# Performance work log

Measured on AMD Instinct MI355X. Metric: run time of the kernel, lower is better.

## Reference

```python
import jax, jax.numpy as jnp
import numpy as np

BN_EPS = 1e-5


def _gru(x, Wih, Whh, bih, bhh):
    # x: [B,S,D]; Wih: [3H,D]; Whh: [3H,H]; PyTorch gate order (r, z, n)
    B, S, D = x.shape
    H = Whh.shape[1]
    xg = jnp.einsum('bsd,gd->bsg', x, Wih) + bih  # [B,S,3H] precomputed input gates

    def step(h, xg_t):
        hg = h @ Whh.T + bhh
        xr, xz, xn = jnp.split(xg_t, 3, axis=-1)
        hr, hz, hn = jnp.split(hg, 3, axis=-1)
        r = jax.nn.sigmoid(xr + hr)
        z = jax.nn.sigmoid(xz + hz)
        n = jnp.tanh(xn + r * hn)
        h_new = (1.0 - z) * n + z * h
        return h_new, h_new

    h0 = jnp.zeros((B, H), x.dtype)
    _, hs = jax.lax.scan(step, h0, jnp.swapaxes(xg, 0, 1))  # [S,B,H]
    return jnp.swapaxes(hs, 0, 1)


def _lstm(x, Wih, Whh, bih, bhh):
    # x: [B,S,D]; PyTorch gate order (i, f, g, o)
    B, S, D = x.shape
    H = Whh.shape[1]
    xg = jnp.einsum('bsd,gd->bsg', x, Wih) + bih  # [B,S,4H]

    def step(carry, xg_t):
        h, c = carry
        g = xg_t + h @ Whh.T + bhh
        i, f, gg, o = jnp.split(g, 4, axis=-1)
        i = jax.nn.sigmoid(i)
        f = jax.nn.sigmoid(f)
        gg = jnp.tanh(gg)
        o = jax.nn.sigmoid(o)
        c_new = f * c + i * gg
        h_new = o * jnp.tanh(c_new)
        return (h_new, c_new), h_new

    h0 = jnp.zeros((B, H), x.dtype)
    c0 = jnp.zeros((B, H), x.dtype)
    _, hs = jax.lax.scan(step, (h0, c0), jnp.swapaxes(xg, 0, 1))
    return jnp.swapaxes(hs, 0, 1)


def setup_inputs() -> dict:
    key = jax.random.key(0)
    B, S, D, H = 64, 512, 40, 512
    ks = jax.random.split(key, 16)
    s_in = 1.0 / np.sqrt(H)

    def u(k, shape):
        return jax.random.uniform(k, shape, jnp.float32, -s_in, s_in)

    inp = {
        'x': jax.random.normal(ks[0], (B, S, D), jnp.float32),
        # rec1: GRU
        'gru_Wih': u(ks[1], (3 * H, D)),
        'gru_Whh': u(ks[2], (3 * H, H)),
        'gru_bih': u(ks[3], (3 * H,)),
        'gru_bhh': u(ks[4], (3 * H,)),
        # rec2: LSTM over [x, ssr] -> input D+1
        'lstm_Wih': u(ks[5], (4 * H, D + 1)),
        'lstm_Whh': u(ks[6], (4 * H, H)),
        'lstm_bih': u(ks[7], (4 * H,)),
        'lstm_bhh': u(ks[8], (4 * H,)),
        # fc1/fc2/fc3: hidden -> 1
        'fc1_w': u(ks[9], (1, H)), 'fc1_b': u(ks[10], (1,)),
        'fc2_w': u(ks[11], (1, H)), 'fc2_b': u(ks[12], (1,)),
        'fc3_w': u(ks[13], (1, H)), 'fc3_b': u(ks[14], (1,)),
        # BatchNorm1d affine params
        'bn_gamma': jnp.ones((H,), jnp.float32),
        'bn_beta': jnp.zeros((H,), jnp.float32),
    }
    return inp


def reference(x, gru_Wih, gru_Whh, gru_bih, gru_bhh,
              lstm_Wih, lstm_Whh, lstm_bih, lstm_bhh,
              fc1_w, fc1_b, fc2_w, fc2_b, fc3_w, fc3_b,
              bn_gamma, bn_beta):
    B, S, D = x.shape
    o1 = _gru(x, gru_Wih, gru_Whh, gru_bih, gru_bhh)  # [B,S,H]
    # BatchNorm1d (training mode): per-channel stats over (batch, time)
    mean = jnp.mean(o1, axis=(0, 1))
    var = jnp.mean((o1 - mean) ** 2, axis=(0, 1))
    o1 = (o1 - mean) * jax.lax.rsqrt(var + BN_EPS) * bn_gamma + bn_beta
    # gated scalar channel (dropout p=0 is identity)
    sr = jax.nn.relu(o1 @ fc1_w.T + fc1_b)            # [B,S,1]
    w = jnp.abs(jax.nn.sigmoid(o1 @ fc2_w.T + fc2_b))  # [B,S,1]
    ssr = sr * (w + 1.0)                              # [B,S,1]
    x2 = jnp.concatenate([x, ssr], axis=2)            # [B,S,D+1]
    o2 = _lstm(x2, lstm_Wih, lstm_Whh, lstm_bih, lstm_bhh)
    out = jax.nn.relu(o2 @ fc3_w.T + fc3_b)           # [B,S,1]
    return out, ssr
```

## Files before the change

### kernel.cpp

```cpp
#include <hip/hip_runtime.h>
#include <stdint.h>

#define MB 16
#define GW 16
#define NU 32
#define HD 512
#define SEQ 512
#define DX 40

using short8 = __attribute__((ext_vector_type(8))) short;
using f32x4  = __attribute__((ext_vector_type(4))) float;
typedef unsigned long long ull;

__device__ __forceinline__ unsigned short f2bf(float f) {
  uint32_t u = __builtin_bit_cast(uint32_t, f);
  u += 0x7fffu + ((u >> 16) & 1u);
  return (unsigned short)(u >> 16);
}
__device__ __forceinline__ float sigm(float x) { return 1.0f / (1.0f + __expf(-x)); }


__global__ __launch_bounds__(512, 2) void gru_kernel(
    const float* __restrict__ x, const float* __restrict__ Wih,
    const float* __restrict__ Whh, const float* __restrict__ bih,
    const float* __restrict__ bhh, unsigned* __restrict__ flags,
    unsigned short* __restrict__ hbuf, float* __restrict__ o1,
    float* __restrict__ stats)
{
  const int wg = blockIdx.x & (GW - 1);
  const int g  = blockIdx.x >> 4;
  const int tid = threadIdx.x;
  const int wave = tid >> 6;
  const int lane = tid & 63;
  const int u0 = wg * NU;
  const int bg = g * MB;

  __shared__ __attribute__((aligned(16))) unsigned short h_s[MB][520];
  __shared__ __attribute__((aligned(16))) unsigned short x_s[MB][72];
  __shared__ float gate_s[3][MB][NU];
  __shared__ float xn_s[MB][NU];

  for (int i = tid; i < MB * 32; i += 512) x_s[i >> 5][40 + (i & 31)] = 0;

  short8 bfrag[18];
  const int myGate = wave >> 1;
  const int ut = wave & 1;
  const int kq = (lane >> 4) * 8;
  if (wave < 6) {
    const int row = myGate * HD + u0 + ut * 16 + (lane & 15);
    for (int kt = 0; kt < 16; ++kt) {
      const float* p = Whh + (size_t)row * HD + kt * 32 + kq;
      short8 f;
#pragma unroll
      for (int j = 0; j < 8; ++j) f[j] = (short)f2bf(p[j]);
      bfrag[kt] = f;
    }
    for (int kt = 16; kt < 18; ++kt) {
      short8 f;
#pragma unroll
      for (int j = 0; j < 8; ++j) {
        int c = kt * 32 + kq + j - HD;
        float v = (myGate < 2 && c < DX) ? Wih[(size_t)row * DX + c] : 0.0f;
        f[j] = (short)f2bf(v);
      }
      bfrag[kt] = f;
    }
  } else {
    const int row = 2 * HD + u0 + (wave - 6) * 16 + (lane & 15);
    for (int kt = 0; kt < 2; ++kt) {
      short8 f;
#pragma unroll
      for (int j = 0; j < 8; ++j) {
        int c = kt * 32 + kq + j;
        f[j] = (short)((c < DX) ? f2bf(Wih[(size_t)row * DX + c]) : 0);
      }
      bfrag[kt] = f;
    }
  }

  const int sb = tid >> 5;
  const int su = tid & 31;
  const int cb = tid & 31;
  float hprev = 0.0f, ssum = 0.0f, ssq = 0.0f;
  const float b_r  = bih[u0 + su] + bhh[u0 + su];
  const float b_z  = bih[HD + u0 + su] + bhh[HD + u0 + su];
  const float b_in = bih[2 * HD + u0 + su];
  const float b_hn = bhh[2 * HD + u0 + su];

  unsigned* gflags = flags + g * 128 * 16;
  unsigned* myflag = gflags + (wg * 8 + wave) * 16;
  unsigned* pollflag = gflags + (((cb >> 1) * 8) + (sb >> 1)) * 16;

  for (int t = 0; t < SEQ; ++t) {
    const ull* hin64 = (const ull*)(hbuf + ((size_t)g * 2 + (t & 1)) * MB * HD);
    uint32_t* hout32 =
        (uint32_t*)(hbuf + ((size_t)g * 2 + ((t + 1) & 1)) * MB * HD);

    const float* xr = x + ((size_t)(bg + sb) * SEQ + t) * DX;
    float xv0 = xr[su];
    float xv1 = (su < 8) ? xr[32 + su] : 0.0f;

    {
      int spin = 0;
      while (__hip_atomic_load(pollflag, __ATOMIC_RELAXED,
                               __HIP_MEMORY_SCOPE_AGENT) < (unsigned)t)
        if (++spin > 2) __builtin_amdgcn_s_sleep(1);
      ull w0 = __hip_atomic_load(hin64 + sb * 128 + cb * 4 + 0, __ATOMIC_RELAXED,
                                 __HIP_MEMORY_SCOPE_AGENT);
      ull w1 = __hip_atomic_load(hin64 + sb * 128 + cb * 4 + 1, __ATOMIC_RELAXED,
                                 __HIP_MEMORY_SCOPE_AGENT);
      ull w2 = __hip_atomic_load(hin64 + sb * 128 + cb * 4 + 2, __ATOMIC_RELAXED,
                                 __HIP_MEMORY_SCOPE_AGENT);
      ull w3 = __hip_atomic_load(hin64 + sb * 128 + cb * 4 + 3, __ATOMIC_RELAXED,
                                 __HIP_MEMORY_SCOPE_AGENT);
      *(ull*)(&h_s[sb][cb * 16 + 0])  = w0;
      *(ull*)(&h_s[sb][cb * 16 + 4])  = w1;
      *(ull*)(&h_s[sb][cb * 16 + 8])  = w2;
      *(ull*)(&h_s[sb][cb * 16 + 12]) = w3;
    }
    x_s[sb][su] = f2bf(xv0);
    if (su < 8) x_s[sb][32 + su] = f2bf(xv1);
    __syncthreads();

    if (wave < 6) {
      const int m = lane & 15;
      f32x4 acc = {0.f, 0.f, 0.f, 0.f};
#pragma unroll
      for (int kt = 0; kt < 16; ++kt) {
        short8 av = *(const short8*)(&h_s[m][kt * 32 + kq]);
        acc = __builtin_amdgcn_mfma_f32_16x16x32_bf16(av, bfrag[kt], acc, 0, 0, 0);
      }
      short8 ax0 = *(const short8*)(&x_s[m][kq]);
      short8 ax1 = *(const short8*)(&x_s[m][32 + kq]);
      acc = __builtin_amdgcn_mfma_f32_16x16x32_bf16(ax0, bfrag[16], acc, 0, 0, 0);
      acc = __builtin_amdgcn_mfma_f32_16x16x32_bf16(ax1, bfrag[17], acc, 0, 0, 0);
#pragma unroll
      for (int r = 0; r < 4; ++r)
        gate_s[myGate][(lane >> 4) * 4 + r][ut * 16 + (lane & 15)] = acc[r];
    } else {
      const int m = lane & 15;
      f32x4 acc = {0.f, 0.f, 0.f, 0.f};
      short8 ax0 = *(const short8*)(&x_s[m][kq]);
      short8 ax1 = *(const short8*)(&x_s[m][32 + kq]);
      acc = __builtin_amdgcn_mfma_f32_16x16x32_bf16(ax0, bfrag[0], acc, 0, 0, 0);
      acc = __builtin_amdgcn_mfma_f32_16x16x32_bf16(ax1, bfrag[1], acc, 0, 0, 0);
#pragma unroll
      for (int r = 0; r < 4; ++r)
        xn_s[(lane >> 4) * 4 + r][(wave - 6) * 16 + (lane & 15)] = acc[r];
    }
    __syncthreads();

    float r_ = sigm(gate_s[0][sb][su] + b_r);
    float z_ = sigm(gate_s[1][sb][su] + b_z);
    float n_ = tanhf(xn_s[sb][su] + b_in + r_ * (gate_s[2][sb][su] + b_hn));
    float h = (1.0f - z_) * n_ + z_ * hprev;
    hprev = h;
    ssum += h; ssq += h * h;
    {
      float hp = __shfl_xor(h, 1);
      if ((tid & 1) == 0) {
        uint32_t packed = (uint32_t)f2bf(h) | ((uint32_t)f2bf(hp) << 16);
        __hip_atomic_store(hout32 + ((sb * HD + u0 + su) >> 1), packed,
                           __ATOMIC_RELAXED, __HIP_MEMORY_SCOPE_AGENT);
      }
      asm volatile("s_waitcnt vmcnt(0)" ::: "memory");
      if (lane == 0)
        __hip_atomic_store(myflag, (unsigned)(t + 1), __ATOMIC_RELAXED,
                           __HIP_MEMORY_SCOPE_AGENT);
    }
    o1[((size_t)(bg + sb) * SEQ + t) * HD + u0 + su] = h;
  }

  atomicAdd(&stats[u0 + su], ssum);
  atomicAdd(&stats[HD + u0 + su], ssq);
}

__global__ __launch_bounds__(512, 2) void lstm_kernel(
    const float* __restrict__ x, const float* __restrict__ Wih,
    const float* __restrict__ Whh, const float* __restrict__ bih,
    const float* __restrict__ bhh, const float* __restrict__ ssr,
    unsigned* __restrict__ flags, unsigned short* __restrict__ hbuf,
    float* __restrict__ o2)
{
  const int wg = blockIdx.x & (GW - 1);
  const int g  = blockIdx.x >> 4;
  const int tid = threadIdx.x;
  const int wave = tid >> 6;
  const int lane = tid & 63;
  const int u0 = wg * NU;
  const int bg = g * MB;

  __shared__ __attribute__((aligned(16))) unsigned short h_s[MB][520];
  __shared__ __attribute__((aligned(16))) unsigned short x_s[MB][72];
  __shared__ float gate_s[4][MB][NU];

  for (int i = tid; i < MB * 23; i += 512) x_s[i / 23][41 + (i % 23)] = 0;

  short8 bfrag[18];
  const int myGate = wave >> 1;
  const int ut = wave & 1;
  const int kq = (lane >> 4) * 8;
  {
    const int row = myGate * HD + u0 + ut * 16 + (lane & 15);
    for (int kt = 0; kt < 16; ++kt) {
      const float* p = Whh + (size_t)row * HD + kt * 32 + kq;
      short8 f;
#pragma unroll
      for (int j = 0; j < 8; ++j) f[j] = (short)f2bf(p[j]);
      bfrag[kt] = f;
    }
    for (int kt = 16; kt < 18; ++kt) {
      short8 f;
#pragma unroll
      for (int j = 0; j < 8; ++j) {
        int c = kt * 32 + kq + j - HD;
        float v = (c < 41) ? Wih[(size_t)row * 41 + c] : 0.0f;
        f[j] = (short)f2bf(v);
      }
      bfrag[kt] = f;
    }
  }

  const int sb = tid >> 5;
  const int su = tid & 31;
  const int cb = tid & 31;
  float creg = 0.0f;
  const float b_i = bih[u0 + su] + bhh[u0 + su];
  const float b_f = bih[HD + u0 + su] + bhh[HD + u0 + su];
  const float b_g = bih[2 * HD + u0 + su] + bhh[2 * HD + u0 + su];
  const float b_o = bih[3 * HD + u0 + su] + bhh[3 * HD + u0 + su];

  unsigned* gflags = flags + g * 128 * 16;
  unsigned* myflag = gflags + (wg * 8 + wave) * 16;
  unsigned* pollflag = gflags + (((cb >> 1) * 8) + (sb >> 1)) * 16;

  for (int t = 0; t < SEQ; ++t) {
    const ull* hin64 = (const ull*)(hbuf + ((size_t)g * 2 + (t & 1)) * MB * HD);
    uint32_t* hout32 =
        (uint32_t*)(hbuf + ((size_t)g * 2 + ((t + 1) & 1)) * MB * HD);

    const float* xr = x + ((size_t)(bg + sb) * SEQ + t) * DX;
    float xv0 = xr[su];
    float xv1 = (su < 8) ? xr[32 + su] : 0.0f;
    float sv = (su == 8) ? ssr[(size_t)(bg + sb) * SEQ + t] : 0.0f;

    {
      int spin = 0;
      while (__hip_atomic_load(pollflag, __ATOMIC_RELAXED,
                               __HIP_MEMORY_SCOPE_AGENT) < (unsigned)t)
        if (++spin > 2) __builtin_amdgcn_s_sleep(1);
      ull w0 = __hip_atomic_load(hin64 + sb * 128 + cb * 4 + 0, __ATOMIC_RELAXED,
                                 __HIP_MEMORY_SCOPE_AGENT);
      ull w1 = __hip_atomic_load(hin64 + sb * 128 + cb * 4 + 1, __ATOMIC_RELAXED,
                                 __HIP_MEMORY_SCOPE_AGENT);
      ull w2 = __hip_atomic_load(hin64 + sb * 128 + cb * 4 + 2, __ATOMIC_RELAXED,
                                 __HIP_MEMORY_SCOPE_AGENT);
      ull w3 = __hip_atomic_load(hin64 + sb * 128 + cb * 4 + 3, __ATOMIC_RELAXED,
                                 __HIP_MEMORY_SCOPE_AGENT);
      *(ull*)(&h_s[sb][cb * 16 + 0])  = w0;
      *(ull*)(&h_s[sb][cb * 16 + 4])  = w1;
      *(ull*)(&h_s[sb][cb * 16 + 8])  = w2;
      *(ull*)(&h_s[sb][cb * 16 + 12]) = w3;
    }
    x_s[sb][su] = f2bf(xv0);
    if (su < 8) x_s[sb][32 + su] = f2bf(xv1);
    if (su == 8) x_s[sb][40] = f2bf(sv);
    __syncthreads();

    {
      const int m = lane & 15;
      f32x4 acc = {0.f, 0.f, 0.f, 0.f};
#pragma unroll
      for (int kt = 0; kt < 16; ++kt) {
        short8 av = *(const short8*)(&h_s[m][kt * 32 + kq]);
        acc = __builtin_amdgcn_mfma_f32_16x16x32_bf16(av, bfrag[kt], acc, 0, 0, 0);
      }
      short8 ax0 = *(const short8*)(&x_s[m][kq]);
      short8 ax1 = *(const short8*)(&x_s[m][32 + kq]);
      acc = __builtin_amdgcn_mfma_f32_16x16x32_bf16(ax0, bfrag[16], acc, 0, 0, 0);
      acc = __builtin_amdgcn_mfma_f32_16x16x32_bf16(ax1, bfrag[17], acc, 0, 0, 0);
#pragma unroll
      for (int r = 0; r < 4; ++r)
        gate_s[myGate][(lane >> 4) * 4 + r][ut * 16 + (lane & 15)] = acc[r];
    }
    __syncthreads();

    float gi = sigm(gate_s[0][sb][su] + b_i);
    float gf_ = sigm(gate_s[1][sb][su] + b_f);
    float gg = tanhf(gate_s[2][sb][su] + b_g);
    float go = sigm(gate_s[3][sb][su] + b_o);
    creg = gf_ * creg + gi * gg;
    float h = go * tanhf(creg);
    {
      float hp = __shfl_xor(h, 1);
      if ((tid & 1) == 0) {
        uint32_t packed = (uint32_t)f2bf(h) | ((uint32_t)f2bf(hp) << 16);
        __hip_atomic_store(hout32 + ((sb * HD + u0 + su) >> 1), packed,
                           __ATOMIC_RELAXED, __HIP_MEMORY_SCOPE_AGENT);
      }
      asm volatile("s_waitcnt vmcnt(0)" ::: "memory");
      if (lane == 0)
        __hip_atomic_store(myflag, (unsigned)(t + 1), __ATOMIC_RELAXED,
                           __HIP_MEMORY_SCOPE_AGENT);
    }
    o2[((size_t)(bg + sb) * SEQ + t) * HD + u0 + su] = h;
  }
}

__global__ __launch_bounds__(512) void coef_kernel(
    const float* __restrict__ stats, const float* __restrict__ fc1_w,
    const float* __restrict__ fc1_b, const float* __restrict__ fc2_w,
    const float* __restrict__ fc2_b, const float* __restrict__ gamma,
    const float* __restrict__ beta, float* __restrict__ coef)
{
  __shared__ float r1[512], r2[512];
  const int j = threadIdx.x;
  const float inv_n = 1.0f / 32768.0f;
  float mean = stats[j] * inv_n;
  float var = stats[HD + j] * inv_n - mean * mean;
  float scale = gamma[j] * rsqrtf(var + 1e-5f);
  float shift = beta[j] - mean * scale;
  coef[j] = fc1_w[j] * scale;
  coef[HD + j] = fc2_w[j] * scale;
  r1[j] = fc1_w[j] * shift;
  r2[j] = fc2_w[j] * shift;
  __syncthreads();
  for (int s = 256; s > 0; s >>= 1) {
    if (j < s) { r1[j] += r1[j + s]; r2[j] += r2[j + s]; }
    __syncthreads();
  }
  if (j == 0) {
    coef[2 * HD] = r1[0] + fc1_b[0];
    coef[2 * HD + 1] = r2[0] + fc2_b[0];
  }
}

__global__ __launch_bounds__(256) void ssr_kernel(
    const float* __restrict__ o1, const float* __restrict__ coef,
    float* __restrict__ ssr_ws, float* __restrict__ dssr)
{
  const int row = blockIdx.x * 4 + (threadIdx.x >> 6);
  const int lane = threadIdx.x & 63;
  const float* p = o1 + (size_t)row * HD + lane * 8;
  float s1 = 0.f, s2 = 0.f;
#pragma unroll
  for (int j = 0; j < 8; ++j) {
    float v = p[j];
    s1 += v * coef[lane * 8 + j];
    s2 += v * coef[HD + lane * 8 + j];
  }
#pragma unroll
  for (int off = 32; off > 0; off >>= 1) {
    s1 += __shfl_down(s1, off);
    s2 += __shfl_down(s2, off);
  }
  if (lane == 0) {
    float sr = fmaxf(s1 + coef[2 * HD], 0.0f);
    float w = fabsf(sigm(s2 + coef[2 * HD + 1]));
    float v = sr * (1.0f + w);
    ssr_ws[row] = v;
    dssr[row] = v;
  }
}

__global__ __launch_bounds__(256) void out_kernel(
    const float* __restrict__ o2, const float* __restrict__ fc3_w,
    const float* __restrict__ fc3_b, float* __restrict__ dout)
{
  const int row = blockIdx.x * 4 + (threadIdx.x >> 6);
  const int lane = threadIdx.x & 63;
  const float* p = o2 + (size_t)row * HD + lane * 8;
  float s = 0.f;
#pragma unroll
  for (int j = 0; j < 8; ++j) s += p[j] * fc3_w[lane * 8 + j];
#pragma unroll
  for (int off = 32; off > 0; off >>= 1) s += __shfl_down(s, off);
  if (lane == 0) dout[row] = fmaxf(s + fc3_b[0], 0.0f);
}

extern "C" void kernel_launch(void* const* d_in, const int* in_sizes, int n_in,
                              void* d_out, int out_size, void* d_ws, size_t ws_size,
                              hipStream_t stream) {
  (void)in_sizes; (void)n_in; (void)out_size; (void)ws_size;
  const float* x    = (const float*)d_in[0];
  const float* gWih = (const float*)d_in[1];
  const float* gWhh = (const float*)d_in[2];
  const float* gbih = (const float*)d_in[3];
  const float* gbhh = (const float*)d_in[4];
  const float* lWih = (const float*)d_in[5];
  const float* lWhh = (const float*)d_in[6];
  const float* lbih = (const float*)d_in[7];
  const float* lbhh = (const float*)d_in[8];
  const float* fc1w = (const float*)d_in[9];
  const float* fc1b = (const float*)d_in[10];
  const float* fc2w = (const float*)d_in[11];
  const float* fc2b = (const float*)d_in[12];
  const float* fc3w = (const float*)d_in[13];
  const float* fc3b = (const float*)d_in[14];
  const float* gam  = (const float*)d_in[15];
  const float* bet  = (const float*)d_in[16];
  float* out = (float*)d_out;

  char* ws = (char*)d_ws;
  unsigned* flags_g = (unsigned*)(ws + 0);
  unsigned* flags_l = (unsigned*)(ws + 32768);
  float* stats      = (float*)(ws + 65536);
  float* coef       = (float*)(ws + 73728);
  float* ssr_ws     = (float*)(ws + 81920);
  unsigned short* hbuf_g = (unsigned short*)(ws + 262144);
  unsigned short* hbuf_l = (unsigned short*)(ws + 393216);
  float* o1 = (float*)(ws + 1048576);
  float* o2 = o1 + (size_t)64 * SEQ * HD;

  hipMemsetAsync(ws, 0, 69632, stream);
  hipMemsetAsync(ws + 262144, 0, 262144, stream);

  gru_kernel<<<dim3(64), dim3(512), 0, stream>>>(x, gWih, gWhh, gbih, gbhh,
                                                 flags_g, hbuf_g, o1, stats);
  coef_kernel<<<dim3(1), dim3(512), 0, stream>>>(stats, fc1w, fc1b, fc2w, fc2b,
                                                 gam, bet, coef);
  ssr_kernel<<<dim3(8192), dim3(256), 0, stream>>>(o1, coef, ssr_ws, out + 32768);
  lstm_kernel<<<dim3(64), dim3(512), 0, stream>>>(x, lWih, lWhh, lbih, lbhh, ssr_ws,
                                                  flags_l, hbuf_l, o2);
  out_kernel<<<dim3(8192), dim3(256), 0, stream>>>(o2, fc3w, fc3b, out);
}
```

Baseline: 3.315 ms.

## Embed timestep tags in hidden-state words to replace separate flag synchronization

The hidden-state exchange buffer now holds 64-bit words that pair two bf16 values with the timestep that wrote them. Consumers spin on the data itself and check that every tag is current. This removes the separate flag store, the vmcnt(0) drain before it, and the flag-poll round trip on each recurrent step. The cost is twice the exchange traffic and wider polling loads, since each lane reads eight 64-bit words per retry.

New measurement: 3.675 ms. +10.9%, slower.

```diff
diff --git a/kernel.cpp b/kernel.cpp
--- a/kernel.cpp
+++ b/kernel.cpp
@@ -7,9 +7,11 @@
 #define HD 512
 #define SEQ 512
 #define DX 40
+#define SLOTW 4096
 
 using short8 = __attribute__((ext_vector_type(8))) short;
 using f32x4  = __attribute__((ext_vector_type(4))) float;
+typedef __attribute__((ext_vector_type(4))) unsigned int u32x4;
 typedef unsigned long long ull;
 
 __device__ __forceinline__ unsigned short f2bf(float f) {
@@ -23,9 +25,8 @@
 __global__ __launch_bounds__(512, 2) void gru_kernel(
     const float* __restrict__ x, const float* __restrict__ Wih,
     const float* __restrict__ Whh, const float* __restrict__ bih,
-    const float* __restrict__ bhh, unsigned* __restrict__ flags,
-    unsigned short* __restrict__ hbuf, float* __restrict__ o1,
-    float* __restrict__ stats)
+    const float* __restrict__ bhh, ull* __restrict__ hbuf,
+    float* __restrict__ o1, float* __restrict__ stats)
 {
   const int wg = blockIdx.x & (GW - 1);
   const int g  = blockIdx.x >> 4;
@@ -87,36 +88,36 @@
   const float b_in = bih[2 * HD + u0 + su];
   const float b_hn = bhh[2 * HD + u0 + su];
 
-  unsigned* gflags = flags + g * 128 * 16;
-  unsigned* myflag = gflags + (wg * 8 + wave) * 16;
-  unsigned* pollflag = gflags + (((cb >> 1) * 8) + (sb >> 1)) * 16;
-
   for (int t = 0; t < SEQ; ++t) {
-    const ull* hin64 = (const ull*)(hbuf + ((size_t)g * 2 + (t & 1)) * MB * HD);
-    uint32_t* hout32 =
-        (uint32_t*)(hbuf + ((size_t)g * 2 + ((t + 1) & 1)) * MB * HD);
+    const ull* in64 = hbuf + ((size_t)g * 2 + (t & 1)) * SLOTW;
+    ull* out64      = hbuf + ((size_t)g * 2 + ((t + 1) & 1)) * SLOTW;
 
     const float* xr = x + ((size_t)(bg + sb) * SEQ + t) * DX;
     float xv0 = xr[su];
     float xv1 = (su < 8) ? xr[32 + su] : 0.0f;
 
     {
+      const ull* hb = in64 + sb * 256 + cb * 8;
+      ull w[8];
       int spin = 0;
-      while (__hip_atomic_load(pollflag, __ATOMIC_RELAXED,
-                               __HIP_MEMORY_SCOPE_AGENT) < (unsigned)t)
+      for (;;) {
+#pragma unroll
+        for (int i = 0; i < 8; ++i)
+          w[i] = __hip_atomic_load(hb + i, __ATOMIC_RELAXED,
+                                   __HIP_MEMORY_SCOPE_AGENT);
+        unsigned mn = (unsigned)(w[0] >> 32);
+#pragma unroll
+        for (int i = 1; i < 8; ++i) {
+          unsigned tg = (unsigned)(w[i] >> 32);
+          mn = (tg < mn) ? tg : mn;
+        }
+        if (mn >= (unsigned)t) break;
         if (++spin > 2) __builtin_amdgcn_s_sleep(1);
-      ull w0 = __hip_atomic_load(hin64 + sb * 128 + cb * 4 + 0, __ATOMIC_RELAXED,
-                                 __HIP_MEMORY_SCOPE_AGENT);
-      ull w1 = __hip_atomic_load(hin64 + sb * 128 + cb * 4 + 1, __ATOMIC_RELAXED,
-                                 __HIP_MEMORY_SCOPE_AGENT);
-      ull w2 = __hip_atomic_load(hin64 + sb * 128 + cb * 4 + 2, __ATOMIC_RELAXED,
-                                 __HIP_MEMORY_SCOPE_AGENT);
-      ull w3 = __hip_atomic_load(hin64 + sb * 128 + cb * 4 + 3, __ATOMIC_RELAXED,
-                                 __HIP_MEMORY_SCOPE_AGENT);
-      *(ull*)(&h_s[sb][cb * 16 + 0])  = w0;
-      *(ull*)(&h_s[sb][cb * 16 + 4])  = w1;
-      *(ull*)(&h_s[sb][cb * 16 + 8])  = w2;
-      *(ull*)(&h_s[sb][cb * 16 + 12]) = w3;
+      }
+      u32x4 lo0 = {(uint32_t)w[0], (uint32_t)w[1], (uint32_t)w[2], (uint32_t)w[3]};
+      u32x4 lo1 = {(uint32_t)w[4], (uint32_t)w[5], (uint32_t)w[6], (uint32_t)w[7]};
+      *(u32x4*)(&h_s[sb][cb * 16 + 0]) = lo0;
+      *(u32x4*)(&h_s[sb][cb * 16 + 8]) = lo1;
     }
     x_s[sb][su] = f2bf(xv0);
     if (su < 8) x_s[sb][32 + su] = f2bf(xv1);
@@ -159,14 +160,11 @@
     {
       float hp = __shfl_xor(h, 1);
       if ((tid & 1) == 0) {
-        uint32_t packed = (uint32_t)f2bf(h) | ((uint32_t)f2bf(hp) << 16);
-        __hip_atomic_store(hout32 + ((sb * HD + u0 + su) >> 1), packed,
+        uint32_t pair = (uint32_t)f2bf(h) | ((uint32_t)f2bf(hp) << 16);
+        ull word = (ull)pair | ((ull)(unsigned)(t + 1) << 32);
+        __hip_atomic_store(out64 + sb * 256 + ((u0 + su) >> 1), word,
                            __ATOMIC_RELAXED, __HIP_MEMORY_SCOPE_AGENT);
       }
-      asm volatile("s_waitcnt vmcnt(0)" ::: "memory");
-      if (lane == 0)
-        __hip_atomic_store(myflag, (unsigned)(t + 1), __ATOMIC_RELAXED,
-                           __HIP_MEMORY_SCOPE_AGENT);
     }
     o1[((size_t)(bg + sb) * SEQ + t) * HD + u0 + su] = h;
   }
@@ -179,8 +177,7 @@
     const float* __restrict__ x, const float* __restrict__ Wih,
     const float* __restrict__ Whh, const float* __restrict__ bih,
     const float* __restrict__ bhh, const float* __restrict__ ssr,
-    unsigned* __restrict__ flags, unsigned short* __restrict__ hbuf,
-    float* __restrict__ o2)
+    ull* __restrict__ hbuf, float* __restrict__ o2)
 {
   const int wg = blockIdx.x & (GW - 1);
   const int g  = blockIdx.x >> 4;
@@ -230,14 +227,9 @@
   const float b_g = bih[2 * HD + u0 + su] + bhh[2 * HD + u0 + su];
   const float b_o = bih[3 * HD + u0 + su] + bhh[3 * HD + u0 + su];
 
-  unsigned* gflags = flags + g * 128 * 16;
-  unsigned* myflag = gflags + (wg * 8 + wave) * 16;
-  unsigned* pollflag = gflags + (((cb >> 1) * 8) + (sb >> 1)) * 16;
-
   for (int t = 0; t < SEQ; ++t) {
-    const ull* hin64 = (const ull*)(hbuf + ((size_t)g * 2 + (t & 1)) * MB * HD);
-    uint32_t* hout32 =
-        (uint32_t*)(hbuf + ((size_t)g * 2 + ((t + 1) & 1)) * MB * HD);
+    const ull* in64 = hbuf + ((size_t)g * 2 + (t & 1)) * SLOTW;
+    ull* out64      = hbuf + ((size_t)g * 2 + ((t + 1) & 1)) * SLOTW;
 
     const float* xr = x + ((size_t)(bg + sb) * SEQ + t) * DX;
     float xv0 = xr[su];
@@ -245,22 +237,27 @@
     float sv = (su == 8) ? ssr[(size_t)(bg + sb) * SEQ + t] : 0.0f;
 
     {
+      const ull* hb = in64 + sb * 256 + cb * 8;
+      ull w[8];
       int spin = 0;
-      while (__hip_atomic_load(pollflag, __ATOMIC_RELAXED,
-                               __HIP_MEMORY_SCOPE_AGENT) < (unsigned)t)
+      for (;;) {
+#pragma unroll
+        for (int i = 0; i < 8; ++i)
+          w[i] = __hip_atomic_load(hb + i, __ATOMIC_RELAXED,
+                                   __HIP_MEMORY_SCOPE_AGENT);
+        unsigned mn = (unsigned)(w[0] >> 32);
+#pragma unroll
+        for (int i = 1; i < 8; ++i) {
+          unsigned tg = (unsigned)(w[i] >> 32);
+          mn = (tg < mn) ? tg : mn;
+        }
+        if (mn >= (unsigned)t) break;
         if (++spin > 2) __builtin_amdgcn_s_sleep(1);
-      ull w0 = __hip_atomic_load(hin64 + sb * 128 + cb * 4 + 0, __ATOMIC_RELAXED,
-                                 __HIP_MEMORY_SCOPE_AGENT);
-      ull w1 = __hip_atomic_load(hin64 + sb * 128 + cb * 4 + 1, __ATOMIC_RELAXED,
-                                 __HIP_MEMORY_SCOPE_AGENT);
-      ull w2 = __hip_atomic_load(hin64 + sb * 128 + cb * 4 + 2, __ATOMIC_RELAXED,
-                                 __HIP_MEMORY_SCOPE_AGENT);
-      ull w3 = __hip_atomic_load(hin64 + sb * 128 + cb * 4 + 3, __ATOMIC_RELAXED,
-                                 __HIP_MEMORY_SCOPE_AGENT);
-      *(ull*)(&h_s[sb][cb * 16 + 0])  = w0;
-      *(ull*)(&h_s[sb][cb * 16 + 4])  = w1;
-      *(ull*)(&h_s[sb][cb * 16 + 8])  = w2;
-      *(ull*)(&h_s[sb][cb * 16 + 12]) = w3;
+      }
+      u32x4 lo0 = {(uint32_t)w[0], (uint32_t)w[1], (uint32_t)w[2], (uint32_t)w[3]};
+      u32x4 lo1 = {(uint32_t)w[4], (uint32_t)w[5], (uint32_t)w[6], (uint32_t)w[7]};
+      *(u32x4*)(&h_s[sb][cb * 16 + 0]) = lo0;
+      *(u32x4*)(&h_s[sb][cb * 16 + 8]) = lo1;
     }
     x_s[sb][su] = f2bf(xv0);
     if (su < 8) x_s[sb][32 + su] = f2bf(xv1);
@@ -294,14 +291,11 @@
     {
       float hp = __shfl_xor(h, 1);
       if ((tid & 1) == 0) {
-        uint32_t packed = (uint32_t)f2bf(h) | ((uint32_t)f2bf(hp) << 16);
-        __hip_atomic_store(hout32 + ((sb * HD + u0 + su) >> 1), packed,
+        uint32_t pair = (uint32_t)f2bf(h) | ((uint32_t)f2bf(hp) << 16);
+        ull word = (ull)pair | ((ull)(unsigned)(t + 1) << 32);
+        __hip_atomic_store(out64 + sb * 256 + ((u0 + su) >> 1), word,
                            __ATOMIC_RELAXED, __HIP_MEMORY_SCOPE_AGENT);
       }
-      asm volatile("s_waitcnt vmcnt(0)" ::: "memory");
-      if (lane == 0)
-        __hip_atomic_store(myflag, (unsigned)(t + 1), __ATOMIC_RELAXED,
-                           __HIP_MEMORY_SCOPE_AGENT);
     }
     o2[((size_t)(bg + sb) * SEQ + t) * HD + u0 + su] = h;
   }
@@ -402,25 +396,23 @@
   float* out = (float*)d_out;
 
   char* ws = (char*)d_ws;
-  unsigned* flags_g = (unsigned*)(ws + 0);
-  unsigned* flags_l = (unsigned*)(ws + 32768);
-  float* stats      = (float*)(ws + 65536);
-  float* coef       = (float*)(ws + 73728);
-  float* ssr_ws     = (float*)(ws + 81920);
-  unsigned short* hbuf_g = (unsigned short*)(ws + 262144);
-  unsigned short* hbuf_l = (unsigned short*)(ws + 393216);
+  float* stats  = (float*)(ws + 65536);
+  float* coef   = (float*)(ws + 73728);
+  float* ssr_ws = (float*)(ws + 81920);
+  ull* hbuf_g = (ull*)(ws + 262144);
+  ull* hbuf_l = (ull*)(ws + 524288);
   float* o1 = (float*)(ws + 1048576);
   float* o2 = o1 + (size_t)64 * SEQ * HD;
 
-  hipMemsetAsync(ws, 0, 69632, stream);
-  hipMemsetAsync(ws + 262144, 0, 262144, stream);
+  hipMemsetAsync(ws + 65536, 0, 4096, stream);
+  hipMemsetAsync(ws + 262144, 0, 524288, stream);
 
   gru_kernel<<<dim3(64), dim3(512), 0, stream>>>(x, gWih, gWhh, gbih, gbhh,
-                                                 flags_g, hbuf_g, o1, stats);
+                                                 hbuf_g, o1, stats);
   coef_kernel<<<dim3(1), dim3(512), 0, stream>>>(stats, fc1w, fc1b, fc2w, fc2b,
                                                  gam, bet, coef);
   ssr_kernel<<<dim3(8192), dim3(256), 0, stream>>>(o1, coef, ssr_ws, out + 32768);
   lstm_kernel<<<dim3(64), dim3(512), 0, stream>>>(x, lWih, lWhh, lbih, lbhh, ssr_ws,
-                                                  flags_l, hbuf_l, o2);
+                                                  hbuf_l, o2);
   out_kernel<<<dim3(8192), dim3(256), 0, stream>>>(o2, fc3w, fc3b, out);
 }
```
